# Performance work log

Hardware: AMD Instinct MI355X
Metric: run time of the kernel (lower is better)

Reference implementation:

```python
import jax, jax.numpy as jnp
import numpy as np

# PiGNNLayer(d_emb=128, n_heads=1, n_neighbors=30); N nodes, E = N*K edges, BSZ graphs
N, K, H, D = 16384, 30, 1, 128
E = N * K
DH = D // H  # d_head
BSZ = 1      # batch_idx is all zeros (see notes: gating broadcast requires bsz==1)


def setup_inputs() -> dict:
    key = jax.random.key(0)
    ks = jax.random.split(key, 16)

    def W(k, i, o):
        return jax.random.normal(k, (i, o), jnp.float32) / np.float32(np.sqrt(i))

    inp = {
        "h": jax.random.normal(ks[0], (N, D), jnp.float32),
        "e": jax.random.normal(ks[1], (E, D), jnp.float32),
        # att_mlp: Linear(3D,D) ReLU Linear(D,D) ReLU Linear(D,H)
        "aw1": W(ks[2], 3 * D, D), "ab1": jnp.zeros((D,), jnp.float32),
        "aw2": W(ks[3], D, D),     "ab2": jnp.zeros((D,), jnp.float32),
        "aw3": W(ks[4], D, H),     "ab3": jnp.zeros((H,), jnp.float32),
        # node_mlp: Linear(2D,D) GELU Linear(D,D) GELU Linear(D,D)
        "nw1": W(ks[5], 2 * D, D), "nb1": jnp.zeros((D,), jnp.float32),
        "nw2": W(ks[6], D, D),     "nb2": jnp.zeros((D,), jnp.float32),
        "nw3": W(ks[7], D, D),     "nb3": jnp.zeros((D,), jnp.float32),
        # to_h: Linear(D, D, bias=False)
        "thw": W(ks[8], H * D, D),
        # gate_mlp: Linear(D,D) ReLU Linear(D,D) ReLU Linear(D,D)
        "gw1": W(ks[9], D, D),  "gb1": jnp.zeros((D,), jnp.float32),
        "gw2": W(ks[10], D, D), "gb2": jnp.zeros((D,), jnp.float32),
        "gw3": W(ks[11], D, D), "gb3": jnp.zeros((D,), jnp.float32),
        # edge_idx[0] = source node i repeated K times (required by '(i j)' reshape)
        "edge_idx": jnp.stack([
            jnp.repeat(jnp.arange(N, dtype=jnp.int32), K),
            jax.random.randint(ks[12], (E,), 0, N, dtype=jnp.int32),
        ]),
        "batch_idx": jnp.zeros((N,), jnp.int32),
    }
    return inp


def reference(h, e, aw1, ab1, aw2, ab2, aw3, ab3,
              nw1, nb1, nw2, nb2, nw3, nb3, thw,
              gw1, gb1, gw2, gb2, gw3, gb3,
              edge_idx, batch_idx):
    src, dst = edge_idx[0], edge_idx[1]
    hi, hj = h[src], h[dst]                       # [E, D] gathers
    cat3 = jnp.concatenate([hi, e, hj], axis=-1)  # [E, 3D]
    cat2 = jnp.concatenate([e, hj], axis=-1)      # [E, 2D]

    # attention logits per head, grouped (i j) -> [H, N, K]
    w = jax.nn.relu(cat3 @ aw1 + ab1)
    w = jax.nn.relu(w @ aw2 + ab2)
    w = (w @ aw3 + ab3)                           # [E, H]
    w = jnp.transpose(w.reshape(N, K, H), (2, 0, 1)) / jnp.sqrt(jnp.float32(DH))
    att = jax.nn.softmax(w, axis=-1)              # softmax over neighbors j

    # values per edge (exact GELU, matching torch nn.GELU default)
    v = jax.nn.gelu(cat2 @ nw1 + nb1, approximate=False)
    v = jax.nn.gelu(v @ nw2 + nb2, approximate=False)
    v = (v @ nw3 + nb3).reshape(N, K, D)          # [N, K, D]

    hh = jnp.einsum('hij,ijd->ihd', att, v).reshape(N, H * D)  # 'h i d -> i (h d)'
    hh = hh @ thw                                 # to_h (no bias)

    # scatter_mean over batch (segment-sum form of the dense-mask trick)
    csum = jax.ops.segment_sum(hh, batch_idx, num_segments=BSZ)
    cnt = jax.ops.segment_sum(jnp.ones((N, 1), hh.dtype), batch_idx, num_segments=BSZ)
    c = csum / cnt                                # [BSZ, D]

    g = jax.nn.relu(c @ gw1 + gb1)
    g = jax.nn.relu(g @ gw2 + gb2)
    g = jax.nn.sigmoid(g @ gw3 + gb3)             # [BSZ, D]
    return hh * g[batch_idx]                      # per-node gate gather
```

## Files before the change

kernel.cpp:

```cpp
#include <hip/hip_runtime.h>
#include <math.h>

#define NN 16384
#define KNB 30
#define NE (NN*KNB)

typedef __attribute__((ext_vector_type(8))) __bf16 bf16x8;
typedef __attribute__((ext_vector_type(4))) float f32x4;
typedef unsigned short ushortT;
typedef __attribute__((ext_vector_type(8))) unsigned short ushort8v;

#define SWZ(r) (((r)&7)<<4)

__device__ __forceinline__ ushortT f2bf(float x){
  __bf16 b = (__bf16)x;
  union { __bf16 b; ushortT u; } v; v.b = b; return v.u;
}
__device__ __forceinline__ float bf2f(ushortT u){
  union { unsigned int u32; float f; } v; v.u32 = ((unsigned int)u) << 16;
  return v.f;
}
__device__ __forceinline__ float bf2f_lo(unsigned int w){
  union { unsigned int u32; float f; } v; v.u32 = w << 16; return v.f;
}
__device__ __forceinline__ float bf2f_hi(unsigned int w){
  union { unsigned int u32; float f; } v; v.u32 = w & 0xffff0000u; return v.f;
}
__device__ __forceinline__ float gelu_f(float x){
  float ax = fabsf(x) * 0.7071067811865476f;
  float t = 1.0f / (1.0f + 0.47047f * ax);
  float poly = t*(0.3480242f + t*(-0.0958798f + t*0.7478556f));
  float er = 1.0f - poly * __expf(-ax*ax);
  er = copysignf(er, x);
  return 0.5f * x * (1.0f + er);
}

__global__ void prep_kernel(const float* __restrict__ h,
                            const float* __restrict__ aw1, const float* __restrict__ nw1,
                            const float* __restrict__ aw2, const float* __restrict__ nw2,
                            const float* __restrict__ nw3, const float* __restrict__ nb3,
                            const float* __restrict__ thw,
                            const float* __restrict__ ab1, const float* __restrict__ nb1,
                            const float* __restrict__ ab2, const float* __restrict__ nb2,
                            ushortT* __restrict__ WF1, ushortT* __restrict__ WF2,
                            float* __restrict__ bias1, float* __restrict__ bias2,
                            float* __restrict__ U, ushortT* __restrict__ WVhP,
                            float* __restrict__ M, float* __restrict__ c3)
{
  __shared__ float sbuf[8*128];
  int tid = threadIdx.x;
  int b = blockIdx.x;

  if (b < 2048) {
    size_t n0 = (size_t)b * 8;
    if (tid < 256) {
      int r = tid >> 5, c = (tid & 31) * 4;
      *(float4*)&sbuf[r*128 + c] = *(const float4*)(h + (n0 + r)*128 + c);
    }
    __syncthreads();
    int d = tid & 127, seg = tid >> 7;
    const float* wbase = (seg == 0) ? (aw1 + d)
                       : (seg == 1) ? (aw1 + 256*128 + d)
                                    : (nw1 + 128*128 + d);
    float s[8] = {0.f,0.f,0.f,0.f,0.f,0.f,0.f,0.f};
    for (int c = 0; c < 128; ++c) {
      float w = wbase[(size_t)c*128];
      #pragma unroll
      for (int r = 0; r < 8; ++r) s[r] += sbuf[r*128 + c] * w;
    }
    if (seg == 0) {
      #pragma unroll
      for (int r = 0; r < 8; ++r) U[(n0 + r)*128 + d] = s[r];
    } else {
      int g = seg - 1;
      int idx = ((g*4 + (d >> 5))*16 + (d & 15))*2 + ((d >> 4) & 1);
      #pragma unroll
      for (int r = 0; r < 8; ++r) WVhP[(n0 + r)*256 + idx] = f2bf(s[r]);
    }
    return;
  }
  if (b < 2107) {
    if (tid >= 256) return;
    int u = (b - 2048) * 256 + tid;
    if (u < 8192) {
      int lane = u & 63, tile = u >> 6;
      int half = tile >> 6, nt = (tile >> 3) & 7, kt = tile & 7;
      int mrow = lane & 15, krow = lane >> 4;
      int n = half*128 + nt*16 + mrow, k0 = kt*32 + krow*8;
      ushort8v o;
      #pragma unroll
      for (int j = 0; j < 8; ++j) {
        int k = k0 + j;
        float v = (half == 0) ? aw1[(128 + k)*128 + n] : nw1[k*128 + (n - 128)];
        o[j] = f2bf(v);
      }
      *(ushort8v*)(WF1 + (size_t)u*8) = o;
      return;
    }
    u -= 8192;
    if (u < 4096) {
      int lane = u & 63, tile = u >> 6;
      int half = tile >> 5, nt = (tile >> 2) & 7, kt = tile & 3;
      int mrow = lane & 15, krow = lane >> 4;
      int n = half*128 + nt*16 + mrow, k0 = kt*32 + krow*8;
      ushort8v o;
      #pragma unroll
      for (int j = 0; j < 8; ++j) {
        int k = k0 + j;
        float v = (half == 0) ? aw2[k*128 + n] : nw2[k*128 + (n - 128)];
        o[j] = f2bf(v);
      }
      *(ushort8v*)(WF2 + (size_t)u*8) = o;
      return;
    }
    u -= 4096;
    if (u < 256) { bias1[u] = (u < 128) ? ab1[u] : nb1[u - 128]; return; }
    u -= 256;
    if (u < 256) { bias2[u] = (u < 128) ? ab2[u] : nb2[u - 128]; return; }
    return;
  }
  {
    if (tid >= 128) return;
    int bb = b - 2107;
    int d = tid;
    sbuf[d] = (bb < 128) ? nw3[bb*128 + d] : nb3[d];
    __syncthreads();
    float s = 0.f;
    for (int n = 0; n < 128; ++n) s += sbuf[n] * thw[n*128 + d];
    if (bb < 128) M[bb*128 + d] = s;
    else c3[d] = s;
  }
}

__global__ __launch_bounds__(512, 8) void edge_kernel(
    const float* __restrict__ e,
    const int* __restrict__ edge_idx,
    const ushortT* __restrict__ WVhP,
    const ushortT* __restrict__ WF1, const ushortT* __restrict__ WF2,
    const float* __restrict__ bias1, const float* __restrict__ bias2,
    const float* __restrict__ aw3, const float* __restrict__ ab3,
    float* __restrict__ hh)
{
  extern __shared__ char smem[];
  char*  Xb   = smem;
  char*  Yb   = smem + 16384;
  float* lgp  = (float*)(smem + 32768);
  float* Ubs  = (float*)(smem + 33280);

  const int tid  = threadIdx.x;
  const int lane = tid & 63;
  const int wid  = tid >> 6;
  const int node = blockIdx.x;
  const long e0 = (long)node * KNB;

  const int mrow = lane & 15, krow = lane >> 4;
  const int wr = wid >> 2;
  const int wq = wid & 3;
  const int row = wr*16 + mrow;

  float uval = 0.f;
  if (tid < 128) uval = hh[(size_t)node*128 + tid];

  int dstr[4];
  #pragma unroll
  for (int rr = 0; rr < 4; ++rr) {
    int orow = wr*16 + krow*4 + rr;
    dstr[rr] = (orow < KNB) ? edge_idx[NE + e0 + orow] : -1;
  }

  {
    int r = tid >> 4, c8 = tid & 15;
    ushort8v u = {0,0,0,0,0,0,0,0};
    if (r < KNB) {
      const float* src = e + ((size_t)(e0 + r))*128 + c8*8;
      float4 v0 = *(const float4*)src;
      float4 v1 = *(const float4*)(src + 4);
      u[0]=f2bf(v0.x); u[1]=f2bf(v0.y); u[2]=f2bf(v0.z); u[3]=f2bf(v0.w);
      u[4]=f2bf(v1.x); u[5]=f2bf(v1.y); u[6]=f2bf(v1.z); u[7]=f2bf(v1.w);
    }
    *(ushort8v*)(Xb + r*512 + ((c8*16) ^ SWZ(r))) = u;
  }

  unsigned int wva[4], wvn[4];
  #pragma unroll
  for (int rr = 0; rr < 4; ++rr) {
    wva[rr] = 0u; wvn[rr] = 0u;
    if (dstr[rr] >= 0) {
      const unsigned int* base = (const unsigned int*)(WVhP + (size_t)dstr[rr]*256);
      wva[rr] = base[wq*16 + mrow];
      wvn[rr] = base[64 + wq*16 + mrow];
    }
  }
  if (tid < 128) Ubs[tid] = uval;
  asm volatile("s_waitcnt lgkmcnt(0)" ::: "memory");
  __builtin_amdgcn_s_barrier();

  const float b1a0 = bias1[wq*32 + mrow],        b1a1 = bias1[wq*32 + 16 + mrow];
  const float b1n0 = bias1[128 + wq*32 + mrow],  b1n1 = bias1[128 + wq*32 + 16 + mrow];
  const float b2a0 = bias2[wq*32 + mrow],        b2a1 = bias2[wq*32 + 16 + mrow];
  const float b2n0 = bias2[128 + wq*32 + mrow],  b2n1 = bias2[128 + wq*32 + 16 + mrow];
  const float aw3c0 = aw3[wq*32 + mrow]      * 0.08838834764831845f;
  const float aw3c1 = aw3[wq*32 + 16 + mrow] * 0.08838834764831845f;

  f32x4 acc[4];
  #pragma unroll
  for (int nt = 0; nt < 4; ++nt) acc[nt] = (f32x4){0.f,0.f,0.f,0.f};

  #pragma unroll
  for (int kt = 0; kt < 4; ++kt) {
    bf16x8 a = *(const bf16x8*)(Xb + row*512 + ((kt*64 + krow*16) ^ SWZ(row)));
    const ushortT* Ba = WF1 + ((size_t)(wq*2)*8 + kt)*512 + lane*8;
    const ushortT* Bn = WF1 + ((size_t)(8 + wq*2)*8 + kt)*512 + lane*8;
    acc[0] = __builtin_amdgcn_mfma_f32_16x16x32_bf16(a, *(const bf16x8*)Ba, acc[0], 0, 0, 0);
    acc[1] = __builtin_amdgcn_mfma_f32_16x16x32_bf16(a, *(const bf16x8*)(Ba + 8*512), acc[1], 0, 0, 0);
    acc[2] = __builtin_amdgcn_mfma_f32_16x16x32_bf16(a, *(const bf16x8*)Bn, acc[2], 0, 0, 0);
    acc[3] = __builtin_amdgcn_mfma_f32_16x16x32_bf16(a, *(const bf16x8*)(Bn + 8*512), acc[3], 0, 0, 0);
  }

  {
    const float b1u0 = b1a0 + Ubs[wq*32 + mrow];
    const float b1u1 = b1a1 + Ubs[wq*32 + 16 + mrow];
    #pragma unroll
    for (int rr = 0; rr < 4; ++rr) {
      int orow = wr*16 + krow*4 + rr;
      char* yrow = Yb + orow*512;
      int sw = SWZ(orow);
      int ca0 = 2*(wq*32 + mrow),        ca1 = 2*(wq*32 + 16 + mrow);
      float x0 = fmaxf(acc[0][rr] + b1u0 + bf2f_lo(wva[rr]), 0.f);
      float x1 = fmaxf(acc[1][rr] + b1u1 + bf2f_hi(wva[rr]), 0.f);
      *(ushortT*)(yrow + (ca0 ^ sw)) = f2bf(x0);
      *(ushortT*)(yrow + (ca1 ^ sw)) = f2bf(x1);
      float y0 = gelu_f(acc[2][rr] + b1n0 + bf2f_lo(wvn[rr]));
      float y1 = gelu_f(acc[3][rr] + b1n1 + bf2f_hi(wvn[rr]));
      *(ushortT*)(yrow + ((256 + ca0) ^ sw)) = f2bf(y0);
      *(ushortT*)(yrow + ((256 + ca1) ^ sw)) = f2bf(y1);
    }
  }
  __syncthreads();

  #pragma unroll
  for (int nt = 0; nt < 4; ++nt) acc[nt] = (f32x4){0.f,0.f,0.f,0.f};
  #pragma unroll
  for (int kt = 0; kt < 4; ++kt) {
    bf16x8 a0 = *(const bf16x8*)(Yb + row*512 + ((kt*64 + krow*16) ^ SWZ(row)));
    bf16x8 a1 = *(const bf16x8*)(Yb + row*512 + ((256 + kt*64 + krow*16) ^ SWZ(row)));
    const ushortT* Ba = WF2 + ((size_t)(wq*2)*4 + kt)*512 + lane*8;
    const ushortT* Bn = WF2 + ((size_t)(8 + wq*2)*4 + kt)*512 + lane*8;
    acc[0] = __builtin_amdgcn_mfma_f32_16x16x32_bf16(a0, *(const bf16x8*)Ba, acc[0], 0, 0, 0);
    acc[1] = __builtin_amdgcn_mfma_f32_16x16x32_bf16(a0, *(const bf16x8*)(Ba + 4*512), acc[1], 0, 0, 0);
    acc[2] = __builtin_amdgcn_mfma_f32_16x16x32_bf16(a1, *(const bf16x8*)Bn, acc[2], 0, 0, 0);
    acc[3] = __builtin_amdgcn_mfma_f32_16x16x32_bf16(a1, *(const bf16x8*)(Bn + 4*512), acc[3], 0, 0, 0);
  }

  {
    #pragma unroll
    for (int rr = 0; rr < 4; ++rr) {
      int orow = wr*16 + krow*4 + rr;
      int sw = SWZ(orow);
      float lsum = fmaxf(acc[0][rr] + b2a0, 0.f) * aw3c0
                 + fmaxf(acc[1][rr] + b2a1, 0.f) * aw3c1;
      lsum += __shfl_xor(lsum, 1);
      lsum += __shfl_xor(lsum, 2);
      lsum += __shfl_xor(lsum, 4);
      lsum += __shfl_xor(lsum, 8);
      if (mrow == 0) lgp[wq*32 + orow] = lsum;
      char* xrow = Xb + orow*512;
      float y0 = gelu_f(acc[2][rr] + b2n0);
      float y1 = gelu_f(acc[3][rr] + b2n1);
      *(ushortT*)(xrow + ((2*(wq*32 + mrow)) ^ sw)) = f2bf(y0);
      *(ushortT*)(xrow + ((2*(wq*32 + 16 + mrow)) ^ sw)) = f2bf(y1);
    }
  }
  __syncthreads();

  {
    float x = -INFINITY;
    if (lane < KNB)
      x = lgp[lane] + lgp[32 + lane] + lgp[64 + lane] + lgp[96 + lane];
    float m = x;
    #pragma unroll
    for (int off = 16; off >= 1; off >>= 1) m = fmaxf(m, __shfl_xor(m, off));
    float p = (lane < KNB) ? __expf(x - m) : 0.f;
    float ssum = p;
    #pragma unroll
    for (int off = 16; off >= 1; off >>= 1) ssum += __shfl_xor(ssum, off);
    float attv = p / ssum;

    int pr = lane & 7, ks = lane >> 3;
    int col0 = wid*16 + pr*2;
    float s0 = 0.f, s1 = 0.f;
    #pragma unroll
    for (int j = 0; j < 4; ++j) {
      int k2 = ks + 8*j;
      float a = __shfl(attv, k2);
      unsigned int w = *(const unsigned int*)(Xb + k2*512 + ((2*col0) ^ SWZ(k2)));
      s0 += a * bf2f_lo(w);
      s1 += a * bf2f_hi(w);
    }
    s0 += __shfl_xor(s0, 8);  s1 += __shfl_xor(s1, 8);
    s0 += __shfl_xor(s0, 16); s1 += __shfl_xor(s1, 16);
    s0 += __shfl_xor(s0, 32); s1 += __shfl_xor(s1, 32);
    if (lane < 8) {
      float2 o; o.x = s0; o.y = s1;
      *(float2*)(hh + (size_t)node*128 + col0) = o;
    }
  }
}

__global__ void reduce1_kernel(const float* __restrict__ hh, float* __restrict__ p2) {
  int b = blockIdx.x, tid = threadIdx.x;
  int d = tid & 127, half = tid >> 7;
  float s = 0.f;
  const float* base = hh + (size_t)(b*64 + half*32)*128 + d;
  #pragma unroll 4
  for (int i = 0; i < 32; ++i) s += base[(size_t)i*128];
  __shared__ float ps[256];
  ps[tid] = s; __syncthreads();
  if (tid < 128) p2[b*128 + tid] = ps[tid] + ps[tid + 128];
}

__global__ void gate_kernel(const float* __restrict__ p2,
                            const float* __restrict__ M, const float* __restrict__ c3,
                            const float* __restrict__ gw1, const float* __restrict__ gb1,
                            const float* __restrict__ gw2, const float* __restrict__ gb2,
                            const float* __restrict__ gw3, const float* __restrict__ gb3,
                            float* __restrict__ gout) {
  int tid = threadIdx.x;
  int d = tid & 127, half = tid >> 7;
  float s = 0.f;
  for (int i = 0; i < 128; ++i) s += p2[(half*128 + i)*128 + d];
  __shared__ float ps[256];
  __shared__ float cv[128], cv2[128], y1[128], y2[128];
  ps[tid] = s; __syncthreads();
  if (tid < 128) cv[tid] = (ps[tid] + ps[tid+128]) * (1.f / (float)NN);
  __syncthreads();
  if (tid < 128) {
    float a = c3[tid];
    for (int c = 0; c < 128; ++c) a += cv[c] * M[c*128 + tid];
    cv2[tid] = a;
  }
  __syncthreads();
  if (tid < 128) {
    float a = gb1[tid];
    for (int c = 0; c < 128; ++c) a += cv2[c] * gw1[c*128 + tid];
    y1[tid] = fmaxf(a, 0.f);
  }
  __syncthreads();
  if (tid < 128) {
    float a = gb2[tid];
    for (int c = 0; c < 128; ++c) a += y1[c] * gw2[c*128 + tid];
    y2[tid] = fmaxf(a, 0.f);
  }
  __syncthreads();
  if (tid < 128) {
    float a = gb3[tid];
    for (int c = 0; c < 128; ++c) a += y2[c] * gw3[c*128 + tid];
    gout[tid] = 1.f / (1.f + __expf(-a));
  }
}

__global__ void toh_scale_kernel(float* __restrict__ hh, const float* __restrict__ M,
                                 const float* __restrict__ c3,
                                 const float* __restrict__ gv)
{
  __shared__ float hs[16][128];
  int tid = threadIdx.x;
  size_t n0 = (size_t)blockIdx.x * 16;
  {
    int r = tid >> 4, c = (tid & 15) * 8;
    const float* src = hh + (n0 + r)*128 + c;
    *(float4*)&hs[r][c]     = *(const float4*)src;
    *(float4*)&hs[r][c + 4] = *(const float4*)(src + 4);
  }
  __syncthreads();
  int d = tid & 127, gq = tid >> 7;
  float s[8] = {0.f,0.f,0.f,0.f,0.f,0.f,0.f,0.f};
  for (int c = 0; c < 128; ++c) {
    float w = M[c*128 + d];
    #pragma unroll
    for (int r = 0; r < 8; ++r) s[r] += hs[gq*8 + r][c] * w;
  }
  float gd = gv[d];
  float cd = c3[d];
  #pragma unroll
  for (int r = 0; r < 8; ++r) hh[(n0 + gq*8 + r)*128 + d] = (s[r] + cd) * gd;
}

extern "C" void kernel_launch(void* const* d_in, const int* in_sizes, int n_in,
                              void* d_out, int out_size, void* d_ws, size_t ws_size,
                              hipStream_t stream) {
  const float* h   = (const float*)d_in[0];
  const float* e   = (const float*)d_in[1];
  const float* aw1 = (const float*)d_in[2];
  const float* ab1 = (const float*)d_in[3];
  const float* aw2 = (const float*)d_in[4];
  const float* ab2 = (const float*)d_in[5];
  const float* aw3 = (const float*)d_in[6];
  const float* ab3 = (const float*)d_in[7];
  const float* nw1 = (const float*)d_in[8];
  const float* nb1 = (const float*)d_in[9];
  const float* nw2 = (const float*)d_in[10];
  const float* nb2 = (const float*)d_in[11];
  const float* nw3 = (const float*)d_in[12];
  const float* nb3 = (const float*)d_in[13];
  const float* thw = (const float*)d_in[14];
  const float* gw1 = (const float*)d_in[15];
  const float* gb1 = (const float*)d_in[16];
  const float* gw2 = (const float*)d_in[17];
  const float* gb2 = (const float*)d_in[18];
  const float* gw3 = (const float*)d_in[19];
  const float* gb3 = (const float*)d_in[20];
  const int* edge_idx = (const int*)d_in[21];

  char* ws = (char*)d_ws;
  ushortT* WF1 = (ushortT*)(ws + 0);
  ushortT* WF2 = (ushortT*)(ws + 131072);
  float* bias1 = (float*)(ws + 196608);
  float* bias2 = (float*)(ws + 197632);
  float* p2    = (float*)(ws + 198656);
  float* gout  = (float*)(ws + 329728);
  float* Mw    = (float*)(ws + 330240);
  float* c3w   = (float*)(ws + 395776);
  ushortT* WVhP= (ushortT*)(ws + 396288);
  float* hh    = (float*)d_out;

  prep_kernel<<<2236, 384, 0, stream>>>(h, aw1, nw1, aw2, nw2, nw3, nb3, thw,
                                        ab1, nb1, ab2, nb2,
                                        WF1, WF2, bias1, bias2,
                                        hh, WVhP, Mw, c3w);

  const int SMEM = 33792;
  hipFuncSetAttribute((const void*)edge_kernel,
                      hipFuncAttributeMaxDynamicSharedMemorySize, SMEM);
  edge_kernel<<<NN, 512, SMEM, stream>>>(e, edge_idx, WVhP, WF1, WF2,
                                         bias1, bias2, aw3, ab3, hh);

  reduce1_kernel<<<256, 256, 0, stream>>>(hh, p2);
  gate_kernel<<<1, 256, 0, stream>>>(p2, Mw, c3w, gw1, gb1, gw2, gb2, gw3, gb3, gout);
  toh_scale_kernel<<<NN/16, 256, 0, stream>>>(hh, Mw, c3w, gout);
}
```

Baseline: 319.4 us.

## Re-partition edge-kernel MFMA tiles so each wave owns one column strip for all rows

Each of the 8 waves now computes a 16-column strip across both 16-row M tiles, instead of a 16-row by 32-column block. Each B-fragment loaded from global is now reused across two A tiles, which halves per-wave weight traffic. The per-row WVhP gather changes to an interleaved layout so a single 32-bit load fetches both the attention and value halves for a column. In exchange, A-fragment LDS reads double, the logit partials grow to 8 per edge with a larger lgp buffer, and the extra shared memory could reduce occupancy.

Result: faster. 306.3 us, median of 3 (-4.1%).

```diff
diff --git a/kernel.cpp b/kernel.cpp
--- a/kernel.cpp
+++ b/kernel.cpp
@@ -72,10 +72,9 @@
       #pragma unroll
       for (int r = 0; r < 8; ++r) U[(n0 + r)*128 + d] = s[r];
     } else {
-      int g = seg - 1;
-      int idx = ((g*4 + (d >> 5))*16 + (d & 15))*2 + ((d >> 4) & 1);
-      #pragma unroll
-      for (int r = 0; r < 8; ++r) WVhP[(n0 + r)*256 + idx] = f2bf(s[r]);
+      int off = seg - 1;
+      #pragma unroll
+      for (int r = 0; r < 8; ++r) WVhP[(n0 + r)*256 + 2*d + off] = f2bf(s[r]);
     }
     return;
   }
@@ -145,7 +144,7 @@
   char*  Xb   = smem;
   char*  Yb   = smem + 16384;
   float* lgp  = (float*)(smem + 32768);
-  float* Ubs  = (float*)(smem + 33280);
+  float* Ubs  = (float*)(smem + 33792);
 
   const int tid  = threadIdx.x;
   const int lane = tid & 63;
@@ -154,19 +153,10 @@
   const long e0 = (long)node * KNB;
 
   const int mrow = lane & 15, krow = lane >> 4;
-  const int wr = wid >> 2;
-  const int wq = wid & 3;
-  const int row = wr*16 + mrow;
+  const int ca = wid*16 + mrow;
 
   float uval = 0.f;
   if (tid < 128) uval = hh[(size_t)node*128 + tid];
-
-  int dstr[4];
-  #pragma unroll
-  for (int rr = 0; rr < 4; ++rr) {
-    int orow = wr*16 + krow*4 + rr;
-    dstr[rr] = (orow < KNB) ? edge_idx[NE + e0 + orow] : -1;
-  }
 
   {
     int r = tid >> 4, c8 = tid & 15;
@@ -181,102 +171,106 @@
     *(ushort8v*)(Xb + r*512 + ((c8*16) ^ SWZ(r))) = u;
   }
 
-  unsigned int wva[4], wvn[4];
-  #pragma unroll
-  for (int rr = 0; rr < 4; ++rr) {
-    wva[rr] = 0u; wvn[rr] = 0u;
-    if (dstr[rr] >= 0) {
-      const unsigned int* base = (const unsigned int*)(WVhP + (size_t)dstr[rr]*256);
-      wva[rr] = base[wq*16 + mrow];
-      wvn[rr] = base[64 + wq*16 + mrow];
+  unsigned int wv[8];
+  #pragma unroll
+  for (int g = 0; g < 8; ++g) {
+    int row_ = (g >> 2)*16 + krow*4 + (g & 3);
+    wv[g] = 0u;
+    if (row_ < KNB) {
+      int dst = edge_idx[NE + e0 + row_];
+      wv[g] = ((const unsigned int*)(WVhP + (size_t)dst*256))[ca];
     }
   }
   if (tid < 128) Ubs[tid] = uval;
   asm volatile("s_waitcnt lgkmcnt(0)" ::: "memory");
   __builtin_amdgcn_s_barrier();
 
-  const float b1a0 = bias1[wq*32 + mrow],        b1a1 = bias1[wq*32 + 16 + mrow];
-  const float b1n0 = bias1[128 + wq*32 + mrow],  b1n1 = bias1[128 + wq*32 + 16 + mrow];
-  const float b2a0 = bias2[wq*32 + mrow],        b2a1 = bias2[wq*32 + 16 + mrow];
-  const float b2n0 = bias2[128 + wq*32 + mrow],  b2n1 = bias2[128 + wq*32 + 16 + mrow];
-  const float aw3c0 = aw3[wq*32 + mrow]      * 0.08838834764831845f;
-  const float aw3c1 = aw3[wq*32 + 16 + mrow] * 0.08838834764831845f;
-
-  f32x4 acc[4];
-  #pragma unroll
-  for (int nt = 0; nt < 4; ++nt) acc[nt] = (f32x4){0.f,0.f,0.f,0.f};
+  const float b1a = bias1[ca],       b1n = bias1[128 + ca];
+  const float b2a = bias2[ca],       b2n = bias2[128 + ca];
+  const float aw3c = aw3[ca] * 0.08838834764831845f;
+
+  f32x4 acc[2][2];
+  #pragma unroll
+  for (int mt = 0; mt < 2; ++mt)
+    #pragma unroll
+    for (int j = 0; j < 2; ++j) acc[mt][j] = (f32x4){0.f,0.f,0.f,0.f};
 
   #pragma unroll
   for (int kt = 0; kt < 4; ++kt) {
-    bf16x8 a = *(const bf16x8*)(Xb + row*512 + ((kt*64 + krow*16) ^ SWZ(row)));
-    const ushortT* Ba = WF1 + ((size_t)(wq*2)*8 + kt)*512 + lane*8;
-    const ushortT* Bn = WF1 + ((size_t)(8 + wq*2)*8 + kt)*512 + lane*8;
-    acc[0] = __builtin_amdgcn_mfma_f32_16x16x32_bf16(a, *(const bf16x8*)Ba, acc[0], 0, 0, 0);
-    acc[1] = __builtin_amdgcn_mfma_f32_16x16x32_bf16(a, *(const bf16x8*)(Ba + 8*512), acc[1], 0, 0, 0);
-    acc[2] = __builtin_amdgcn_mfma_f32_16x16x32_bf16(a, *(const bf16x8*)Bn, acc[2], 0, 0, 0);
-    acc[3] = __builtin_amdgcn_mfma_f32_16x16x32_bf16(a, *(const bf16x8*)(Bn + 8*512), acc[3], 0, 0, 0);
-  }
-
-  {
-    const float b1u0 = b1a0 + Ubs[wq*32 + mrow];
-    const float b1u1 = b1a1 + Ubs[wq*32 + 16 + mrow];
-    #pragma unroll
-    for (int rr = 0; rr < 4; ++rr) {
-      int orow = wr*16 + krow*4 + rr;
-      char* yrow = Yb + orow*512;
-      int sw = SWZ(orow);
-      int ca0 = 2*(wq*32 + mrow),        ca1 = 2*(wq*32 + 16 + mrow);
-      float x0 = fmaxf(acc[0][rr] + b1u0 + bf2f_lo(wva[rr]), 0.f);
-      float x1 = fmaxf(acc[1][rr] + b1u1 + bf2f_hi(wva[rr]), 0.f);
-      *(ushortT*)(yrow + (ca0 ^ sw)) = f2bf(x0);
-      *(ushortT*)(yrow + (ca1 ^ sw)) = f2bf(x1);
-      float y0 = gelu_f(acc[2][rr] + b1n0 + bf2f_lo(wvn[rr]));
-      float y1 = gelu_f(acc[3][rr] + b1n1 + bf2f_hi(wvn[rr]));
-      *(ushortT*)(yrow + ((256 + ca0) ^ sw)) = f2bf(y0);
-      *(ushortT*)(yrow + ((256 + ca1) ^ sw)) = f2bf(y1);
-    }
-  }
-  __syncthreads();
-
-  #pragma unroll
-  for (int nt = 0; nt < 4; ++nt) acc[nt] = (f32x4){0.f,0.f,0.f,0.f};
+    int koff = kt*64 + krow*16;
+    bf16x8 a0 = *(const bf16x8*)(Xb + mrow*512 + (koff ^ SWZ(mrow)));
+    bf16x8 a1 = *(const bf16x8*)(Xb + (16 + mrow)*512 + (koff ^ SWZ(16 + mrow)));
+    bf16x8 ba = *(const bf16x8*)(WF1 + ((size_t)(wid*8 + kt))*512 + lane*8);
+    bf16x8 bn = *(const bf16x8*)(WF1 + ((size_t)((8 + wid)*8 + kt))*512 + lane*8);
+    acc[0][0] = __builtin_amdgcn_mfma_f32_16x16x32_bf16(a0, ba, acc[0][0], 0, 0, 0);
+    acc[1][0] = __builtin_amdgcn_mfma_f32_16x16x32_bf16(a1, ba, acc[1][0], 0, 0, 0);
+    acc[0][1] = __builtin_amdgcn_mfma_f32_16x16x32_bf16(a0, bn, acc[0][1], 0, 0, 0);
+    acc[1][1] = __builtin_amdgcn_mfma_f32_16x16x32_bf16(a1, bn, acc[1][1], 0, 0, 0);
+  }
+
+  {
+    const float b1u = b1a + Ubs[ca];
+    #pragma unroll
+    for (int mt = 0; mt < 2; ++mt)
+      #pragma unroll
+      for (int rr = 0; rr < 4; ++rr) {
+        int row_ = mt*16 + krow*4 + rr;
+        int g = mt*4 + rr;
+        char* yrow = Yb + row_*512;
+        int sw = SWZ(row_);
+        float x = fmaxf(acc[mt][0][rr] + b1u + bf2f_lo(wv[g]), 0.f);
+        *(ushortT*)(yrow + ((2*ca) ^ sw)) = f2bf(x);
+        float y = gelu_f(acc[mt][1][rr] + b1n + bf2f_hi(wv[g]));
+        *(ushortT*)(yrow + ((256 + 2*ca) ^ sw)) = f2bf(y);
+      }
+  }
+  __syncthreads();
+
+  #pragma unroll
+  for (int mt = 0; mt < 2; ++mt)
+    #pragma unroll
+    for (int j = 0; j < 2; ++j) acc[mt][j] = (f32x4){0.f,0.f,0.f,0.f};
   #pragma unroll
   for (int kt = 0; kt < 4; ++kt) {
-    bf16x8 a0 = *(const bf16x8*)(Yb + row*512 + ((kt*64 + krow*16) ^ SWZ(row)));
-    bf16x8 a1 = *(const bf16x8*)(Yb + row*512 + ((256 + kt*64 + krow*16) ^ SWZ(row)));
-    const ushortT* Ba = WF2 + ((size_t)(wq*2)*4 + kt)*512 + lane*8;
-    const ushortT* Bn = WF2 + ((size_t)(8 + wq*2)*4 + kt)*512 + lane*8;
-    acc[0] = __builtin_amdgcn_mfma_f32_16x16x32_bf16(a0, *(const bf16x8*)Ba, acc[0], 0, 0, 0);
-    acc[1] = __builtin_amdgcn_mfma_f32_16x16x32_bf16(a0, *(const bf16x8*)(Ba + 4*512), acc[1], 0, 0, 0);
-    acc[2] = __builtin_amdgcn_mfma_f32_16x16x32_bf16(a1, *(const bf16x8*)Bn, acc[2], 0, 0, 0);
-    acc[3] = __builtin_amdgcn_mfma_f32_16x16x32_bf16(a1, *(const bf16x8*)(Bn + 4*512), acc[3], 0, 0, 0);
-  }
-
-  {
-    #pragma unroll
-    for (int rr = 0; rr < 4; ++rr) {
-      int orow = wr*16 + krow*4 + rr;
-      int sw = SWZ(orow);
-      float lsum = fmaxf(acc[0][rr] + b2a0, 0.f) * aw3c0
-                 + fmaxf(acc[1][rr] + b2a1, 0.f) * aw3c1;
-      lsum += __shfl_xor(lsum, 1);
-      lsum += __shfl_xor(lsum, 2);
-      lsum += __shfl_xor(lsum, 4);
-      lsum += __shfl_xor(lsum, 8);
-      if (mrow == 0) lgp[wq*32 + orow] = lsum;
-      char* xrow = Xb + orow*512;
-      float y0 = gelu_f(acc[2][rr] + b2n0);
-      float y1 = gelu_f(acc[3][rr] + b2n1);
-      *(ushortT*)(xrow + ((2*(wq*32 + mrow)) ^ sw)) = f2bf(y0);
-      *(ushortT*)(xrow + ((2*(wq*32 + 16 + mrow)) ^ sw)) = f2bf(y1);
-    }
+    int koff = kt*64 + krow*16;
+    bf16x8 aw0 = *(const bf16x8*)(Yb + mrow*512 + (koff ^ SWZ(mrow)));
+    bf16x8 aw1v = *(const bf16x8*)(Yb + (16 + mrow)*512 + (koff ^ SWZ(16 + mrow)));
+    bf16x8 av0 = *(const bf16x8*)(Yb + mrow*512 + ((256 + koff) ^ SWZ(mrow)));
+    bf16x8 av1 = *(const bf16x8*)(Yb + (16 + mrow)*512 + ((256 + koff) ^ SWZ(16 + mrow)));
+    bf16x8 ba = *(const bf16x8*)(WF2 + ((size_t)(wid*4 + kt))*512 + lane*8);
+    bf16x8 bn = *(const bf16x8*)(WF2 + ((size_t)((8 + wid)*4 + kt))*512 + lane*8);
+    acc[0][0] = __builtin_amdgcn_mfma_f32_16x16x32_bf16(aw0, ba, acc[0][0], 0, 0, 0);
+    acc[1][0] = __builtin_amdgcn_mfma_f32_16x16x32_bf16(aw1v, ba, acc[1][0], 0, 0, 0);
+    acc[0][1] = __builtin_amdgcn_mfma_f32_16x16x32_bf16(av0, bn, acc[0][1], 0, 0, 0);
+    acc[1][1] = __builtin_amdgcn_mfma_f32_16x16x32_bf16(av1, bn, acc[1][1], 0, 0, 0);
+  }
+
+  {
+    #pragma unroll
+    for (int mt = 0; mt < 2; ++mt)
+      #pragma unroll
+      for (int rr = 0; rr < 4; ++rr) {
+        int row_ = mt*16 + krow*4 + rr;
+        int sw = SWZ(row_);
+        float lsum = fmaxf(acc[mt][0][rr] + b2a, 0.f) * aw3c;
+        lsum += __shfl_xor(lsum, 1);
+        lsum += __shfl_xor(lsum, 2);
+        lsum += __shfl_xor(lsum, 4);
+        lsum += __shfl_xor(lsum, 8);
+        if (mrow == 0) lgp[wid*32 + row_] = lsum;
+        float y = gelu_f(acc[mt][1][rr] + b2n);
+        *(ushortT*)(Xb + row_*512 + ((2*ca) ^ sw)) = f2bf(y);
+      }
   }
   __syncthreads();
 
   {
     float x = -INFINITY;
-    if (lane < KNB)
-      x = lgp[lane] + lgp[32 + lane] + lgp[64 + lane] + lgp[96 + lane];
+    if (lane < KNB) {
+      x = lgp[lane];
+      #pragma unroll
+      for (int w = 1; w < 8; ++w) x += lgp[w*32 + lane];
+    }
     float m = x;
     #pragma unroll
     for (int off = 16; off >= 1; off >>= 1) m = fmaxf(m, __shfl_xor(m, off));
@@ -429,7 +423,7 @@
                                         WF1, WF2, bias1, bias2,
                                         hh, WVhP, Mw, c3w);
 
-  const int SMEM = 33792;
+  const int SMEM = 34304;
   hipFuncSetAttribute((const void*)edge_kernel,
                       hipFuncAttributeMaxDynamicSharedMemorySize, SMEM);
   edge_kernel<<<NN, 512, SMEM, stream>>>(e, edge_idx, WVhP, WF1, WF2,
```
